# Kernel optimization log

Measured on AMD Instinct MI355X. Metric: run time of the kernel, lower is better.

The kernel has to match this reference:

```python
import jax, jax.numpy as jnp
import numpy as np

DIM = 1152
HEADS = 9
MID = 256
B, N = 8, 1024


def _conprefix(x, dw, db, uw, ub):
    # torch Linear: y = x @ W.T + b
    kv = jnp.tanh(x @ dw.T + db) @ uw.T + ub  # [B, N, 2*dim]
    q = jnp.zeros(kv.shape[:2] + (DIM,), kv.dtype)
    return jnp.concatenate([q, kv], axis=-1)  # [B, N, 3*dim]


def setup_inputs() -> dict:
    key = jax.random.key(0)
    ks = jax.random.split(key, 12)
    s = 0.02
    return {
        "x": jax.random.normal(ks[0], (B, N, DIM), dtype=jnp.float32),
        "Wqkv": jax.random.normal(ks[1], (3 * DIM, DIM), dtype=jnp.float32) * s,
        "Wproj": jax.random.normal(ks[2], (DIM, DIM), dtype=jnp.float32) * s,
        "bproj": jax.random.normal(ks[3], (DIM,), dtype=jnp.float32) * s,
        "down_w": jax.random.normal(ks[4], (MID, DIM), dtype=jnp.float32) * s,
        "down_b": jax.random.normal(ks[5], (MID,), dtype=jnp.float32) * s,
        "up_w": jax.random.normal(ks[6], (2 * DIM, MID), dtype=jnp.float32) * s,
        "up_b": jax.random.normal(ks[7], (2 * DIM,), dtype=jnp.float32) * s,
        "pdown_w": jax.random.normal(ks[8], (MID, DIM), dtype=jnp.float32) * s,
        "pdown_b": jax.random.normal(ks[9], (MID,), dtype=jnp.float32) * s,
        "pup_w": jax.random.normal(ks[10], (2 * DIM, MID), dtype=jnp.float32) * s,
        "pup_b": jax.random.normal(ks[11], (2 * DIM,), dtype=jnp.float32) * s,
        "task": 5,
    }


def reference(x, Wqkv, Wproj, bproj, down_w, down_b, up_w, up_b,
              pdown_w, pdown_b, pup_w, pup_b, task):
    b, n, c = x.shape
    hd = c // HEADS
    scale = hd ** (-0.5)
    qkv = x @ Wqkv.T  # [B, N, 3C] (qkv_bias=False)
    task_prefix_tensor = None
    if task <= 3:
        pass
    elif task == 4:
        qkv = qkv + _conprefix(x, down_w, down_b, up_w, up_b)
        task_prefix_tensor = down_w
    else:
        qkv = (qkv + _conprefix(x, pdown_w, pdown_b, pup_w, pup_b)
                   + _conprefix(x, down_w, down_b, up_w, up_b))
        task_prefix_tensor = down_w
    qkv = qkv.reshape(b, n, 3, HEADS, hd).transpose(2, 0, 3, 1, 4)  # [3,B,H,N,hd]
    q, k, v = qkv[0], qkv[1], qkv[2]
    attn = jax.nn.softmax(jnp.einsum('bhqd,bhkd->bhqk', q, k) * scale, axis=-1)
    out = jnp.einsum('bhqk,bhkd->bhqd', attn, v)  # [B,H,N,hd]
    out = out.transpose(0, 2, 1, 3).reshape(b, n, c)
    out = out @ Wproj.T + bproj
    return (out, task_prefix_tensor)
```

## Files before the change

### kernel.cpp

```cpp
#include <hip/hip_runtime.h>
#include <math.h>

namespace {

typedef unsigned short u16;
typedef __attribute__((ext_vector_type(8))) short short8;
typedef __attribute__((ext_vector_type(4))) float f32x4;
typedef __attribute__((ext_vector_type(16))) float f32x16;

constexpr int kDim   = 1152;
constexpr int kHeads = 9;
constexpr int kMid   = 256;
constexpr int kB     = 8;
constexpr int kN     = 1024;
constexpr int kM     = kB * kN;
constexpr int kQS    = 3584;
constexpr float kCexp  = 0.12753837360881433f;

__device__ __forceinline__ u16 f2bf(float f) {
    unsigned u = __builtin_bit_cast(unsigned, f);
    return (u16)((u + 0x7FFFu + ((u >> 16) & 1u)) >> 16);
}
__device__ __forceinline__ float bf2f(u16 h) {
    unsigned u = ((unsigned)h) << 16;
    return __builtin_bit_cast(float, u);
}

__device__ __forceinline__ void gload_lds16(const void* g, void* l) {
    __builtin_amdgcn_global_load_lds(
        (const __attribute__((address_space(1))) unsigned int*)g,
        (__attribute__((address_space(3))) unsigned int*)l,
        16, 0, 0);
}

__device__ __forceinline__ unsigned cvtpk(float a, float b) {
    unsigned r;
    asm volatile("v_cvt_pk_bf16_f32 %0, %1, %2" : "=v"(r) : "v"(a), "v"(b));
    return r;
}

__device__ __forceinline__ void halfswap(unsigned& x, unsigned& y, bool hihalf) {
    const unsigned xs = (unsigned)__shfl_xor((int)x, 32);
    const unsigned ys = (unsigned)__shfl_xor((int)y, 32);
    const unsigned nx = hihalf ? ys : x;
    const unsigned ny = hihalf ? y : xs;
    x = nx; y = ny;
}

__device__ __forceinline__ short8 build_pfrag(float p0, float p1, float p2, float p3,
                                              float p4, float p5, float p6, float p7,
                                              bool hihalf) {
    unsigned x1 = cvtpk(p0, p1), y1 = cvtpk(p4, p5);
    unsigned x2 = cvtpk(p2, p3), y2 = cvtpk(p6, p7);
    halfswap(x1, y1, hihalf);
    halfswap(x2, y2, hihalf);
    union { unsigned u[4]; short8 s; } pk;
    pk.u[0] = x1; pk.u[1] = x2; pk.u[2] = y1; pk.u[3] = y2;
    return pk.s;
}

constexpr int R0 = 2359296;
constexpr int R1 = R0 + 995328;
constexpr int R2 = R1 + 331776;
constexpr int R3 = R2 + 73728;
constexpr int R4 = R3 + 73728;
constexpr int R5 = R4 + 147456;
constexpr int R6 = R5 + 147456;
constexpr int R7 = R6 + 512;
constexpr int R8 = R7 + 2304;
constexpr int kQPart = 331776;
constexpr int kPrepGrid = R8 / 256;

__global__ __launch_bounds__(256)
void prep_all(const float* __restrict__ x, const float* __restrict__ Wqkv,
              const float* __restrict__ Wproj,
              const float* __restrict__ down_w, const float* __restrict__ pdown_w,
              const float* __restrict__ up_w, const float* __restrict__ pup_w,
              const float* __restrict__ down_b, const float* __restrict__ pdown_b,
              const float* __restrict__ up_b, const float* __restrict__ pup_b,
              const int* __restrict__ task,
              u16* __restrict__ xb, u16* __restrict__ wqkvb, u16* __restrict__ wprjb,
              u16* __restrict__ wdownb, u16* __restrict__ wupb,
              float* __restrict__ bd, float* __restrict__ bu)
{
    const int i = blockIdx.x * blockDim.x + threadIdx.x;
    auto cvt4s = [](const float* s, int j, float sc) {
        const float4 v = reinterpret_cast<const float4*>(s)[j];
        ushort4 o;
        o.x = f2bf(v.x * sc); o.y = f2bf(v.y * sc);
        o.z = f2bf(v.z * sc); o.w = f2bf(v.w * sc);
        return o;
    };
    if (i < R0) {
        reinterpret_cast<ushort4*>(xb)[i] = cvt4s(x, i, 1.f);
    } else if (i < R1) {
        const int j = i - R0;
        const float sc = (j < kQPart) ? kCexp : 1.f;
        reinterpret_cast<ushort4*>(wqkvb)[j] = cvt4s(Wqkv, j, sc);
    } else if (i < R2) {
        reinterpret_cast<ushort4*>(wprjb)[i - R1] = cvt4s(Wproj, i - R1, 1.f);
    } else if (i < R3) {
        reinterpret_cast<ushort4*>(wdownb)[i - R2] = cvt4s(down_w, i - R2, 1.f);
    } else if (i < R4) {
        reinterpret_cast<ushort4*>(wdownb)[73728 + (i - R3)] = cvt4s(pdown_w, i - R3, 1.f);
    } else if (i < R5) {
        const int j = i - R4, r = j >> 6, c = j & 63;
        reinterpret_cast<ushort4*>(wupb)[r * 128 + c] = cvt4s(up_w, j, 1.f);
    } else if (i < R6) {
        const int j = i - R5, r = j >> 6, c = j & 63;
        reinterpret_cast<ushort4*>(wupb)[r * 128 + 64 + c] = cvt4s(pup_w, j, 1.f);
    } else if (i < R7) {
        const int j = i - R6;
        bd[j] = (j < 256) ? down_b[j] : pdown_b[j - 256];
    } else {
        const int j = i - R7;
        bu[j] = up_b[j] + ((*task >= 5) ? pup_b[j] : 0.f);
    }
}

template<bool ACCUM, bool BIAS, bool KSEL>
__global__ __launch_bounds__(512, 2)
void gemm8p(const u16* __restrict__ A, const u16* __restrict__ Bw,
            const float* __restrict__ bias, u16* __restrict__ C,
            int K, int lda, int ldb, int ldc,
            const int* __restrict__ taskp, int mintask)
{
    if (taskp != nullptr && *taskp < mintask) return;
    if (KSEL && *taskp < 5) K = 256;

    extern __shared__ char lds[];

    const int tid  = threadIdx.x;
    const int lane = tid & 63;
    const int wid  = tid >> 6;
    const int wm   = wid >> 2;
    const int wn   = wid & 3;
    const int bm   = blockIdx.x * 256;
    const int bn   = blockIdx.y * 256;
    const int l15  = lane & 15;
    const int kq   = lane >> 4;

    int srow[4], scol[4], sdst[4];
#pragma unroll
    for (int i = 0; i < 4; ++i) {
        const int id = i * 512 + tid;
        srow[i] = id >> 3;
        const int s = id & 7;
        scol[i] = (s ^ (srow[i] & 7)) * 8;
        sdst[i] = (i * 512 + wid * 64) * 16;
    }

    auto stage_pair = [&](int buf, int kt, int i) {
        const u16* ag = A  + (size_t)bm * lda + kt * 64;
        const u16* bg = Bw + (size_t)bn * ldb + kt * 64;
        gload_lds16(ag + (size_t)srow[i] * lda + scol[i], lds + buf * 32768 + sdst[i]);
        gload_lds16(bg + (size_t)srow[i] * ldb + scol[i], lds + 65536 + buf * 32768 + sdst[i]);
    };

    f32x4 acc[8][4] = {};
    const int nt = K >> 6;

#pragma unroll
    for (int i = 0; i < 4; ++i) stage_pair(0, 0, i);

    for (int t = 0; t < nt; ++t) {
        const char* Ab = lds + (t & 1) * 32768;
        const char* Bb = lds + 65536 + (t & 1) * 32768;
        const bool nxt = (t + 1 < nt);
        const int nb = (t + 1) & 1;

        short8 af[4], bf[4];

        auto rdA = [&](int mh, int ks) {
#pragma unroll
            for (int mi = 0; mi < 4; ++mi) {
                const int row = wm * 128 + mh * 64 + mi * 16 + l15;
                af[mi] = *reinterpret_cast<const short8*>(
                    Ab + row * 128 + (((ks * 4 + kq) ^ (row & 7)) * 16));
            }
        };
        auto rdB = [&](int ks) {
#pragma unroll
            for (int ni = 0; ni < 4; ++ni) {
                const int row = wn * 64 + ni * 16 + l15;
                bf[ni] = *reinterpret_cast<const short8*>(
                    Bb + row * 128 + (((ks * 4 + kq) ^ (row & 7)) * 16));
            }
        };
        auto mfma16 = [&](int mh) {
            asm volatile("s_waitcnt lgkmcnt(0)" ::: "memory");
            __builtin_amdgcn_sched_barrier(0);
            __builtin_amdgcn_s_setprio(1);
#pragma unroll
            for (int mi = 0; mi < 4; ++mi)
#pragma unroll
                for (int ni = 0; ni < 4; ++ni)
                    acc[mh * 4 + mi][ni] = __builtin_amdgcn_mfma_f32_16x16x32_bf16(
                        af[mi], bf[ni], acc[mh * 4 + mi][ni], 0, 0, 0);
            __builtin_amdgcn_s_setprio(0);
            asm volatile("" ::: "memory");
            __builtin_amdgcn_s_barrier();
            asm volatile("" ::: "memory");
        };

        if (nxt) { stage_pair(nb, t + 1, 0); stage_pair(nb, t + 1, 1); }
        if (nxt) asm volatile("s_waitcnt vmcnt(4)" ::: "memory");
        else     asm volatile("s_waitcnt vmcnt(0)" ::: "memory");
        __builtin_amdgcn_sched_barrier(0);
        __builtin_amdgcn_s_barrier();
        asm volatile("" ::: "memory");
        rdB(0); rdA(0, 0);
        mfma16(0);

        if (nxt) { stage_pair(nb, t + 1, 2); stage_pair(nb, t + 1, 3); }
        rdA(1, 0);
        mfma16(1);

        rdB(1); rdA(0, 1);
        mfma16(0);

        rdA(1, 1);
        mfma16(1);
    }

#pragma unroll
    for (int mg = 0; mg < 8; ++mg) {
#pragma unroll
        for (int ni = 0; ni < 4; ++ni) {
            const int col = bn + wn * 64 + ni * 16 + l15;
            const float bv = BIAS ? bias[col] : 0.f;
#pragma unroll
            for (int r = 0; r < 4; ++r) {
                const int row = bm + wm * 128 + mg * 16 + kq * 4 + r;
                float v = acc[mg][ni][r] + bv;
                u16* cp = C + (size_t)row * ldc + col;
                if (ACCUM) v += bf2f(*cp);
                *cp = f2bf(v);
            }
        }
    }
}

template<bool TANH, bool ACCUM, bool BIAS, bool OUT_BF16>
__global__ __launch_bounds__(256)
void gemm_mfma(const u16* __restrict__ A, const u16* __restrict__ Bw,
               const float* __restrict__ bias, void* __restrict__ Cv,
               int K, int lda, int ldb, int ldc,
               const int* __restrict__ taskp, int mintask)
{
    if (taskp != nullptr && *taskp < mintask) return;

    __shared__ u16 As[2][128 * 64];
    __shared__ u16 Bs[2][128 * 64];

    const int tid  = threadIdx.x;
    const int lane = tid & 63;
    const int wv   = tid >> 6;
    const int wr   = (wv >> 1) * 64;
    const int wc   = (wv & 1) * 64;
    const int bm   = blockIdx.x * 128;
    const int bn   = blockIdx.y * 128;

    f32x4 acc[4][4] = {};

    const int srow = tid >> 3;
    const int sslt = tid & 7;

    auto stage = [&](int buf, int k0) {
        const u16* ab = A  + (size_t)bm * lda + k0;
        const u16* bb = Bw + (size_t)bn * ldb + k0;
#pragma unroll
        for (int i = 0; i < 4; ++i) {
            const int row = i * 32 + srow;
            gload_lds16(ab + (size_t)row * lda + sslt * 8,
                        (char*)&As[buf][0] + (i * 256 + (tid & 192)) * 16);
        }
#pragma unroll
        for (int i = 0; i < 4; ++i) {
            const int row = i * 32 + srow;
            gload_lds16(bb + (size_t)row * ldb + sslt * 8,
                        (char*)&Bs[buf][0] + (i * 256 + (tid & 192)) * 16);
        }
    };

    stage(0, 0);
    const int nk = K >> 6;
    for (int kt = 0; kt < nk; ++kt) {
        __syncthreads();
        if (kt + 1 < nk) stage((kt + 1) & 1, (kt + 1) * 64);
        const u16* as = &As[kt & 1][0];
        const u16* bs = &Bs[kt & 1][0];
#pragma unroll
        for (int ks = 0; ks < 2; ++ks) {
            short8 af[4], bf[4];
#pragma unroll
            for (int mi = 0; mi < 4; ++mi) {
                const int row = wr + mi * 16 + (lane & 15);
                af[mi] = *reinterpret_cast<const short8*>(as + row * 64 + ks * 32 + (lane >> 4) * 8);
            }
#pragma unroll
            for (int ni = 0; ni < 4; ++ni) {
                const int row = wc + ni * 16 + (lane & 15);
                bf[ni] = *reinterpret_cast<const short8*>(bs + row * 64 + ks * 32 + (lane >> 4) * 8);
            }
#pragma unroll
            for (int mi = 0; mi < 4; ++mi)
#pragma unroll
                for (int ni = 0; ni < 4; ++ni)
                    acc[mi][ni] = __builtin_amdgcn_mfma_f32_16x16x32_bf16(
                        af[mi], bf[ni], acc[mi][ni], 0, 0, 0);
        }
    }

#pragma unroll
    for (int mi = 0; mi < 4; ++mi) {
#pragma unroll
        for (int ni = 0; ni < 4; ++ni) {
            const int col = bn + wc + ni * 16 + (lane & 15);
            const float bv = BIAS ? bias[col] : 0.f;
#pragma unroll
            for (int r = 0; r < 4; ++r) {
                const int row = bm + wr + mi * 16 + (lane >> 4) * 4 + r;
                float v = acc[mi][ni][r] + bv;
                if (TANH) v = tanhf(v);
                if (OUT_BF16) {
                    u16* cp = (u16*)Cv + (size_t)row * ldc + col;
                    if (ACCUM) v += bf2f(*cp);
                    *cp = f2bf(v);
                } else {
                    float* cp = (float*)Cv + (size_t)row * ldc + col;
                    if (ACCUM) v += *cp;
                    *cp = v;
                }
            }
        }
    }
}

__global__ __launch_bounds__(256)
void transpose_v(const u16* __restrict__ qkv, u16* __restrict__ vt)
{
    __shared__ u16 t[64][136];
    const int bh = blockIdx.x, b = bh / kHeads, h = bh - b * kHeads;
    const int n0 = blockIdx.y * 64;
    const int tid = threadIdx.x;
#pragma unroll
    for (int it = 0; it < 4; ++it) {
        const int I = it * 256 + tid, tok = I >> 4, s = I & 15;
        *reinterpret_cast<short8*>(&t[tok][s * 8]) =
            *reinterpret_cast<const short8*>(
                qkv + (size_t)(b * kN + n0 + tok) * kQS + 2304 + h * 128 + s * 8);
    }
    __syncthreads();
#pragma unroll
    for (int it = 0; it < 8; ++it) {
        const int I = it * 256 + tid;
        const int d = I >> 4, tk = (I & 15) * 4;
        ushort4 v;
        v.x = t[tk + 0][d]; v.y = t[tk + 1][d];
        v.z = t[tk + 2][d]; v.w = t[tk + 3][d];
        *reinterpret_cast<ushort4*>(vt + (size_t)(bh * 128 + d) * kN + n0 + tk) = v;
    }
}

__global__ __launch_bounds__(256)
void attn_mfma(const u16* __restrict__ qkv, const u16* __restrict__ vt,
               u16* __restrict__ out)
{
    __shared__ u16 Ks[64 * 128];
    __shared__ u16 Vs[128 * 64];

    const int bh = blockIdx.x, b = bh / kHeads, h = bh - b * kHeads;
    const int tid = threadIdx.x, lane = tid & 63, wv = tid >> 6;
    const int lo5 = lane & 31;
    const bool hihalf = (lane >= 32);
    const int hi = hihalf ? 1 : 0;
    const int q0 = blockIdx.y * 128 + wv * 32;

    const u16* qp = qkv + (size_t)(b * kN + q0 + lo5) * kQS + h * 128;
    short8 qf[8];
#pragma unroll
    for (int f = 0; f < 8; ++f)
        qf[f] = *reinterpret_cast<const short8*>(qp + f * 16 + hi * 8);

    int koff[4], voff[4];
#pragma unroll
    for (int j = 0; j < 4; ++j) {
        const int I = (wv * 4 + j) * 64 + lane;
        const int tok = I >> 4, s = I & 15;
        koff[j] = tok * kQS + ((s ^ (tok & 7)) * 8);
        const int d = I >> 3, sv = I & 7;
        voff[j] = d * kN + ((sv ^ (d & 7)) * 8);
    }
    const u16* kbase = qkv + (size_t)b * kN * kQS + kDim + h * 128;
    const u16* vbase = vt + (size_t)bh * 128 * kN;

    f32x16 o[4] = {};
    float l = 0.f;

    for (int kt = 0; kt < kN; kt += 64) {
        __syncthreads();
#pragma unroll
        for (int j = 0; j < 4; ++j)
            gload_lds16(kbase + (size_t)kt * kQS + koff[j], (char*)Ks + (wv * 4 + j) * 1024);
#pragma unroll
        for (int j = 0; j < 4; ++j)
            gload_lds16(vbase + kt + voff[j], (char*)Vs + (wv * 4 + j) * 1024);
        __syncthreads();

        f32x16 s0 = {}, s1 = {};
        __builtin_amdgcn_s_setprio(1);
#pragma unroll
        for (int f = 0; f < 8; ++f) {
            const int c = (f * 2 + hi) * 16;
            const int swz = (lo5 & 7) << 4;
            const short8 ka = *reinterpret_cast<const short8*>(
                (const char*)Ks + lo5 * 256 + (c ^ swz));
            const short8 kb = *reinterpret_cast<const short8*>(
                (const char*)Ks + (lo5 + 32) * 256 + (c ^ swz));
            s0 = __builtin_amdgcn_mfma_f32_32x32x16_bf16(ka, qf[f], s0, 0, 0, 0);
            s1 = __builtin_amdgcn_mfma_f32_32x32x16_bf16(kb, qf[f], s1, 0, 0, 0);
        }
        __builtin_amdgcn_s_setprio(0);

        float rsum = 0.f;
#pragma unroll
        for (int r = 0; r < 16; ++r) { s0[r] = exp2f(s0[r]); rsum += s0[r]; }
#pragma unroll
        for (int r = 0; r < 16; ++r) { s1[r] = exp2f(s1[r]); rsum += s1[r]; }
        rsum += __shfl_xor(rsum, 32);
        l += rsum;

        short8 pf[4];
        pf[0] = build_pfrag(s0[0], s0[1], s0[2], s0[3], s0[4], s0[5], s0[6], s0[7], hihalf);
        pf[1] = build_pfrag(s0[8], s0[9], s0[10], s0[11], s0[12], s0[13], s0[14], s0[15], hihalf);
        pf[2] = build_pfrag(s1[0], s1[1], s1[2], s1[3], s1[4], s1[5], s1[6], s1[7], hihalf);
        pf[3] = build_pfrag(s1[8], s1[9], s1[10], s1[11], s1[12], s1[13], s1[14], s1[15], hihalf);

        __builtin_amdgcn_s_setprio(1);
#pragma unroll
        for (int dt = 0; dt < 4; ++dt) {
            const int drow = dt * 32 + lo5;
            const int swz = (lo5 & 7) << 4;
#pragma unroll
            for (int c = 0; c < 4; ++c) {
                const int col = (c * 2 + hi) * 16;
                const short8 va = *reinterpret_cast<const short8*>(
                    (const char*)Vs + drow * 128 + (col ^ swz));
                o[dt] = __builtin_amdgcn_mfma_f32_32x32x16_bf16(va, pf[c], o[dt], 0, 0, 0);
            }
        }
        __builtin_amdgcn_s_setprio(0);
    }

    const float inv = 1.f / l;
    u16* op = out + (size_t)(b * kN + q0 + lo5) * kDim + h * 128;
#pragma unroll
    for (int dt = 0; dt < 4; ++dt) {
#pragma unroll
        for (int rg = 0; rg < 4; ++rg) {
            const int d0 = dt * 32 + rg * 8 + hi * 4;
            ushort4 v;
            v.x = f2bf(o[dt][rg * 4 + 0] * inv);
            v.y = f2bf(o[dt][rg * 4 + 1] * inv);
            v.z = f2bf(o[dt][rg * 4 + 2] * inv);
            v.w = f2bf(o[dt][rg * 4 + 3] * inv);
            *reinterpret_cast<ushort4*>(op + d0) = v;
        }
    }
}

}

extern "C" void kernel_launch(void* const* d_in, const int* in_sizes, int n_in,
                              void* d_out, int out_size, void* d_ws, size_t ws_size,
                              hipStream_t stream)
{
    const float* x       = (const float*)d_in[0];
    const float* Wqkv    = (const float*)d_in[1];
    const float* Wproj   = (const float*)d_in[2];
    const float* bproj   = (const float*)d_in[3];
    const float* down_w  = (const float*)d_in[4];
    const float* down_b  = (const float*)d_in[5];
    const float* up_w    = (const float*)d_in[6];
    const float* up_b    = (const float*)d_in[7];
    const float* pdown_w = (const float*)d_in[8];
    const float* pdown_b = (const float*)d_in[9];
    const float* pup_w   = (const float*)d_in[10];
    const float* pup_b   = (const float*)d_in[11];
    const int*   task    = (const int*)d_in[12];

    u16* xb_vt  = (u16*)d_ws;
    u16* wqkvb  = xb_vt  + (size_t)kM * kDim;
    u16* wprjb  = wqkvb  + (size_t)kQS * kDim;
    u16* wdownb = wprjb  + (size_t)kDim * kDim;
    u16* wupb   = wdownb + (size_t)512 * kDim;
    u16* h12    = wupb   + (size_t)2304 * 512;
    u16* qkvb   = h12    + (size_t)kM * 512;
    u16* aob    = qkvb   + (size_t)kM * kQS;
    float* bd   = (float*)(aob + (size_t)kM * kDim);
    float* bu   = bd + 512;
    float* out  = (float*)d_out;
    u16* xb = xb_vt;
    u16* vt = xb_vt;

    prep_all<<<kPrepGrid, 256, 0, stream>>>(
        x, Wqkv, Wproj, down_w, pdown_w, up_w, pup_w,
        down_b, pdown_b, up_b, pup_b, task,
        xb, wqkvb, wprjb, wdownb, wupb, bd, bu);

    hipFuncSetAttribute(reinterpret_cast<const void*>(&gemm8p<false, false, false>),
                        hipFuncAttributeMaxDynamicSharedMemorySize, 131072);
    hipFuncSetAttribute(reinterpret_cast<const void*>(&gemm8p<true, true, true>),
                        hipFuncAttributeMaxDynamicSharedMemorySize, 131072);

    gemm_mfma<true, false, true, true><<<dim3(kM / 128, 4), 256, 0, stream>>>(
        xb, wdownb, bd, h12, kDim, kDim, kDim, 512, nullptr, 0);
    gemm8p<false, false, false><<<dim3(kM / 256, kQS / 256), 512, 131072, stream>>>(
        xb, wqkvb, nullptr, qkvb, kDim, kDim, kDim, kQS, nullptr, 0);
    gemm8p<true, true, true><<<dim3(kM / 256, 9), 512, 131072, stream>>>(
        h12, wupb, bu, qkvb + kDim, 512, 512, 512, kQS, task, 4);

    transpose_v<<<dim3(kB * kHeads, kN / 64), 256, 0, stream>>>(qkvb, vt);

    attn_mfma<<<dim3(kB * kHeads, kN / 128), 256, 0, stream>>>(qkvb, vt, aob);

    gemm_mfma<false, false, true, false><<<dim3(kM / 128, 9), 256, 0, stream>>>(
        aob, wprjb, bproj, out, kDim, kDim, kDim, kDim, nullptr, 0);

    hipMemcpyAsync(out + (size_t)kM * kDim, down_w,
                   (size_t)kMid * kDim * sizeof(float),
                   hipMemcpyDeviceToDevice, stream);
}
```

Before: 346.0 us.

## Split attention over two key halves and merge partials in a combine kernel

Splits the attention kernel's key loop into two halves along a new grid dimension, doubling the block count. Each half writes unnormalized bf16 partial outputs plus its softmax row sums. A new elementwise kernel adds the two partials and normalizes them. The aim is better CU utilization and less tail imbalance, at the cost of an extra launch, roughly 56 MB of extra partial-output traffic, and extra bf16 rounding of the partials.

New measurement: 349.5 us. Within noise of the previous version (+1.0%).

```diff
diff --git a/kernel.cpp b/kernel.cpp
--- a/kernel.cpp
+++ b/kernel.cpp
@@ -365,12 +365,13 @@
 
 __global__ __launch_bounds__(256)
 void attn_mfma(const u16* __restrict__ qkv, const u16* __restrict__ vt,
-               u16* __restrict__ out)
+               u16* __restrict__ po, float* __restrict__ pl)
 {
     __shared__ u16 Ks[64 * 128];
     __shared__ u16 Vs[128 * 64];
 
     const int bh = blockIdx.x, b = bh / kHeads, h = bh - b * kHeads;
+    const int sp = blockIdx.z;
     const int tid = threadIdx.x, lane = tid & 63, wv = tid >> 6;
     const int lo5 = lane & 31;
     const bool hihalf = (lane >= 32);
@@ -398,7 +399,8 @@
     f32x16 o[4] = {};
     float l = 0.f;
 
-    for (int kt = 0; kt < kN; kt += 64) {
+    const int kt0 = sp * (kN / 2);
+    for (int kt = kt0; kt < kt0 + kN / 2; kt += 64) {
         __syncthreads();
 #pragma unroll
         for (int j = 0; j < 4; ++j)
@@ -453,21 +455,43 @@
         __builtin_amdgcn_s_setprio(0);
     }
 
-    const float inv = 1.f / l;
-    u16* op = out + (size_t)(b * kN + q0 + lo5) * kDim + h * 128;
+    const int row = b * kN + q0 + lo5;
+    u16* op = po + (size_t)sp * kM * kDim + (size_t)row * kDim + h * 128;
 #pragma unroll
     for (int dt = 0; dt < 4; ++dt) {
 #pragma unroll
         for (int rg = 0; rg < 4; ++rg) {
             const int d0 = dt * 32 + rg * 8 + hi * 4;
             ushort4 v;
-            v.x = f2bf(o[dt][rg * 4 + 0] * inv);
-            v.y = f2bf(o[dt][rg * 4 + 1] * inv);
-            v.z = f2bf(o[dt][rg * 4 + 2] * inv);
-            v.w = f2bf(o[dt][rg * 4 + 3] * inv);
+            v.x = f2bf(o[dt][rg * 4 + 0]);
+            v.y = f2bf(o[dt][rg * 4 + 1]);
+            v.z = f2bf(o[dt][rg * 4 + 2]);
+            v.w = f2bf(o[dt][rg * 4 + 3]);
             *reinterpret_cast<ushort4*>(op + d0) = v;
         }
     }
+    if (!hihalf)
+        pl[sp * (kM * kHeads) + row * kHeads + h] = l;
+}
+
+constexpr int kCmbGrid = (kM * kDim / 8) / 256;
+
+__global__ __launch_bounds__(256)
+void attn_combine(const u16* __restrict__ po, const float* __restrict__ pl,
+                  u16* __restrict__ aob)
+{
+    const int i = blockIdx.x * 256 + threadIdx.x;
+    const int row = i / 144;
+    const int g   = i - row * 144;
+    const int h   = g >> 4;
+    const float inv = 1.f / (pl[row * kHeads + h] + pl[kM * kHeads + row * kHeads + h]);
+    const short8 a = reinterpret_cast<const short8*>(po)[i];
+    const short8 c = reinterpret_cast<const short8*>(po + (size_t)kM * kDim)[i];
+    short8 r;
+#pragma unroll
+    for (int j = 0; j < 8; ++j)
+        r[j] = (short)f2bf((bf2f((u16)a[j]) + bf2f((u16)c[j])) * inv);
+    reinterpret_cast<short8*>(aob)[i] = r;
 }
 
 }
@@ -500,6 +524,8 @@
     u16* aob    = qkvb   + (size_t)kM * kQS;
     float* bd   = (float*)(aob + (size_t)kM * kDim);
     float* bu   = bd + 512;
+    u16* po     = (u16*)(bu + 2304);
+    float* pl   = (float*)(po + (size_t)2 * kM * kDim);
     float* out  = (float*)d_out;
     u16* xb = xb_vt;
     u16* vt = xb_vt;
@@ -523,7 +549,8 @@
 
     transpose_v<<<dim3(kB * kHeads, kN / 64), 256, 0, stream>>>(qkvb, vt);
 
-    attn_mfma<<<dim3(kB * kHeads, kN / 128), 256, 0, stream>>>(qkvb, vt, aob);
+    attn_mfma<<<dim3(kB * kHeads, kN / 128, 2), 256, 0, stream>>>(qkvb, vt, po, pl);
+    attn_combine<<<kCmbGrid, 256, 0, stream>>>(po, pl, aob);
 
     gemm_mfma<false, false, true, false><<<dim3(kM / 128, 9), 256, 0, stream>>>(
         aob, wprjb, bproj, out, kDim, kDim, kDim, kDim, nullptr, 0);
```
